# Optimization experiments

Hardware: AMD Instinct MI355X
Metric: run time of the kernel (lower is better)

## Reference

```python
import jax, jax.numpy as jnp
import numpy as np

MARGIN = 0.5


def _pairwise_dist(x):
    # Euclidean cdist via ||a||^2 + ||b||^2 - 2ab, with safe sqrt.
    sq = jnp.sum(x * x, axis=-1)  # (N,)
    d2 = sq[:, None] + sq[None, :] - 2.0 * (x @ x.T)
    d2 = jnp.maximum(d2, 0.0)
    return jnp.sqrt(jnp.where(d2 > 0.0, d2, 1.0)) * (d2 > 0.0)


def setup_inputs() -> dict:
    key = jax.random.key(0)
    k1, k2 = jax.random.split(key)
    N, D = 8192, 128
    embeddings = jax.random.normal(k1, (N, D), dtype=jnp.float32)
    labels = jax.random.randint(k2, (N,), 0, 7, dtype=jnp.int64)
    return {"embeddings": embeddings, "labels": labels}


def reference(embeddings, labels):
    N = embeddings.shape[0]
    dist = _pairwise_dist(embeddings)  # (N, N)
    same = labels[:, None] == labels[None, :]
    eye = jnp.eye(N, dtype=bool)
    pos_mask = same & ~eye
    neg_mask = ~same
    big = jnp.asarray(jnp.finfo(dist.dtype).max, dist.dtype)
    # hardest positive: max dist among same-label (excl. self)
    pos_dist = jnp.max(jnp.where(pos_mask, dist, -big), axis=1)
    # hardest negative: min dist among different-label
    neg_dist = jnp.min(jnp.where(neg_mask, dist, big), axis=1)
    valid = jnp.any(pos_mask, axis=1) & jnp.any(neg_mask, axis=1)
    per_row = jax.nn.relu(pos_dist - neg_dist + MARGIN)
    loss_sum = jnp.sum(jnp.where(valid, per_row, 0.0))
    count = jnp.sum(valid)
    return loss_sum / jnp.maximum(count, 1).astype(loss_sum.dtype)
```

## Files before the change

### kernel.cpp

```cpp
#include <hip/hip_runtime.h>

#define N 8192
#define D 128
#define MARGIN 0.5f
#define FLT_BIG 3.402823466e+38f

typedef __bf16 bf16x8 __attribute__((ext_vector_type(8)));
typedef float f32x4 __attribute__((ext_vector_type(4)));
typedef unsigned short u16x8 __attribute__((ext_vector_type(8)));

__device__ __forceinline__ unsigned short f2bf_rne(float f) {
  unsigned u = __float_as_uint(f);
  u += 0x7FFFu + ((u >> 16) & 1u);
  return (unsigned short)(u >> 16);
}

#define FRAG_OFF(tile, k, lane) ((size_t)(tile) * 2048 + (size_t)(k) * 512 + (size_t)(lane) * 8)

__global__ void k_prep(const float* __restrict__ x, const int* __restrict__ lab,
                       unsigned short* __restrict__ xb, float* __restrict__ sq,
                       unsigned* __restrict__ posw, unsigned* __restrict__ negw,
                       unsigned* __restrict__ hist, float* __restrict__ acc,
                       unsigned* __restrict__ ticket) {
  const int t = threadIdx.x;
  const int row = blockIdx.x * 16 + (t >> 4);
  const int c = t & 15;
  const float4 v0 = ((const float4*)x)[row * 32 + c * 2];
  const float4 v1 = ((const float4*)x)[row * 32 + c * 2 + 1];
  u16x8 o;
  o[0] = f2bf_rne(v0.x); o[1] = f2bf_rne(v0.y);
  o[2] = f2bf_rne(v0.z); o[3] = f2bf_rne(v0.w);
  o[4] = f2bf_rne(v1.x); o[5] = f2bf_rne(v1.y);
  o[6] = f2bf_rne(v1.z); o[7] = f2bf_rne(v1.w);
  *(u16x8*)(xb + FRAG_OFF(row >> 4, c >> 2, ((c & 3) * 16) + (row & 15))) = o;
  float s = v0.x * v0.x + v0.y * v0.y + v0.z * v0.z + v0.w * v0.w +
            v1.x * v1.x + v1.y * v1.y + v1.z * v1.z + v1.w * v1.w;
#pragma unroll
  for (int off = 1; off < 16; off <<= 1) s += __shfl_xor(s, off, 64);
  if (c == 0) {
    sq[row] = s;
    posw[row] = 0u;
    negw[row] = 0x7F800000u;
  }

  if (blockIdx.x == 0) {
    __shared__ unsigned h[8];
    if (t < 8) h[t] = 0u;
    __syncthreads();
    unsigned long long cA = 0ull, cB = 0ull;
#pragma unroll
    for (int it = 0; it < 32; ++it) {
      const int l = lab[t + it * 256] & 7;
      if (l < 4) cA += 1ull << (l * 16);
      else       cB += 1ull << ((l - 4) * 16);
    }
#pragma unroll
    for (int off = 1; off < 64; off <<= 1) {
      cA += __shfl_xor(cA, off, 64);
      cB += __shfl_xor(cB, off, 64);
    }
    if ((t & 63) == 0) {
#pragma unroll
      for (int q = 0; q < 4; ++q) {
        atomicAdd(&h[q],     (unsigned)((cA >> (q * 16)) & 0xFFFFu));
        atomicAdd(&h[4 + q], (unsigned)((cB >> (q * 16)) & 0xFFFFu));
      }
    }
    __syncthreads();
    if (t < 8) hist[t] = h[t];
    if (t == 0) { acc[0] = 0.f; acc[1] = 0.f; ticket[0] = 0u; }
  }
}

__global__ __launch_bounds__(256, 4) void k_mine(
    const unsigned short* __restrict__ xb, const float* __restrict__ sq,
    const int* __restrict__ lab, unsigned* __restrict__ posw, unsigned* __restrict__ negw) {
  const int t = threadIdx.x;
  const int w = t >> 6;
  const int lane = t & 63;
  const int col = lane & 15;
  const int quad = lane >> 4;
  const int i0 = blockIdx.x * 128 + w * 32;
  const int jbase = blockIdx.y * 256;

  bf16x8 a[2][4];
#pragma unroll
  for (int is = 0; is < 2; ++is)
#pragma unroll
    for (int k = 0; k < 4; ++k)
      a[is][k] = *(const bf16x8*)(xb + FRAG_OFF((i0 >> 4) + is, k, lane));

  int labi[2][4];
#pragma unroll
  for (int is = 0; is < 2; ++is)
#pragma unroll
    for (int r = 0; r < 4; ++r) labi[is][r] = lab[i0 + is * 16 + quad * 4 + r];

  float pos[2][4], neg[2][4];
#pragma unroll
  for (int is = 0; is < 2; ++is)
#pragma unroll
    for (int r = 0; r < 4; ++r) { pos[is][r] = -FLT_BIG; neg[is][r] = FLT_BIG; }

  const float* sqp = sq + jbase + col;
  const int* labp = lab + jbase + col;
  const unsigned short* gb = xb + FRAG_OFF(jbase >> 4, 0, lane);

  bf16x8 b0A, b1A, b2A, b3A, b0B, b1B, b2B, b3B;
  float sqjA, sqjB;
  int labjA, labjB;

#define LOADB(S, js_) do {                                        \
    const unsigned short* g = gb + (size_t)(js_) * 2048;          \
    b0##S = *(const bf16x8*)(g);                                  \
    b1##S = *(const bf16x8*)(g + 512);                            \
    b2##S = *(const bf16x8*)(g + 1024);                           \
    b3##S = *(const bf16x8*)(g + 1536);                           \
    sqj##S = sqp[(js_) * 16];                                     \
    labj##S = labp[(js_) * 16];                                   \
  } while (0)

#define COMPUTE(S) do {                                                        \
    f32x4 acc0 = {0.f, 0.f, 0.f, 0.f}, acc1 = {0.f, 0.f, 0.f, 0.f};           \
    acc0 = __builtin_amdgcn_mfma_f32_16x16x32_bf16(a[0][0], b0##S, acc0, 0, 0, 0); \
    acc1 = __builtin_amdgcn_mfma_f32_16x16x32_bf16(a[1][0], b0##S, acc1, 0, 0, 0); \
    acc0 = __builtin_amdgcn_mfma_f32_16x16x32_bf16(a[0][1], b1##S, acc0, 0, 0, 0); \
    acc1 = __builtin_amdgcn_mfma_f32_16x16x32_bf16(a[1][1], b1##S, acc1, 0, 0, 0); \
    acc0 = __builtin_amdgcn_mfma_f32_16x16x32_bf16(a[0][2], b2##S, acc0, 0, 0, 0); \
    acc1 = __builtin_amdgcn_mfma_f32_16x16x32_bf16(a[1][2], b2##S, acc1, 0, 0, 0); \
    acc0 = __builtin_amdgcn_mfma_f32_16x16x32_bf16(a[0][3], b3##S, acc0, 0, 0, 0); \
    acc1 = __builtin_amdgcn_mfma_f32_16x16x32_bf16(a[1][3], b3##S, acc1, 0, 0, 0); \
    _Pragma("unroll")                                                          \
    for (int r = 0; r < 4; ++r) {                                              \
      const float m0 = fmaf(-2.f, acc0[r], sqj##S);                            \
      const float m1 = fmaf(-2.f, acc1[r], sqj##S);                            \
      const bool s0 = (labi[0][r] == labj##S);                                 \
      const bool s1 = (labi[1][r] == labj##S);                                 \
      pos[0][r] = fmaxf(pos[0][r], s0 ? m0 : -FLT_BIG);                        \
      neg[0][r] = fminf(neg[0][r], s0 ? FLT_BIG : m0);                         \
      pos[1][r] = fmaxf(pos[1][r], s1 ? m1 : -FLT_BIG);                        \
      neg[1][r] = fminf(neg[1][r], s1 ? FLT_BIG : m1);                         \
    }                                                                          \
  } while (0)

  LOADB(A, 0);
#pragma unroll 1
  for (int js = 0; js < 14; js += 2) {
    LOADB(B, js + 1);
    COMPUTE(A);
    LOADB(A, js + 2);
    COMPUTE(B);
  }
  LOADB(B, 15);
  COMPUTE(A);
  COMPUTE(B);

#undef LOADB
#undef COMPUTE

#pragma unroll
  for (int is = 0; is < 2; ++is)
#pragma unroll
    for (int r = 0; r < 4; ++r) {
      float p = pos[is][r], n = neg[is][r];
#pragma unroll
      for (int off = 1; off < 16; off <<= 1) {
        p = fmaxf(p, __shfl_xor(p, off, 64));
        n = fminf(n, __shfl_xor(n, off, 64));
      }
      if (col == 0) {
        const int i = i0 + is * 16 + quad * 4 + r;
        const float sqi = sq[i];
        atomicMax(posw + i, __float_as_uint(fmaxf(sqi + p, 0.f)));
        atomicMin(negw + i, __float_as_uint(fmaxf(sqi + n, 0.f)));
      }
    }
}

__global__ void k_tail(const unsigned* __restrict__ posw, const unsigned* __restrict__ negw,
                       const int* __restrict__ lab, const unsigned* __restrict__ hist,
                       float* __restrict__ acc, unsigned* __restrict__ ticket,
                       float* __restrict__ out) {
  __shared__ float ls[4], cs[4];
  const int t = threadIdx.x;
  const int i = blockIdx.x * 256 + t;
  const float pd2 = __uint_as_float(posw[i]);
  const float nd2 = __uint_as_float(negw[i]);
  const unsigned cnt = hist[lab[i] & 7];
  const bool valid = (cnt >= 2u) && (cnt < (unsigned)N);
  float loss = 0.f, c = 0.f;
  if (valid) {
    loss = fmaxf(sqrtf(pd2) - sqrtf(fminf(nd2, FLT_BIG)) + MARGIN, 0.f);
    c = 1.f;
  }
#pragma unroll
  for (int off = 1; off < 64; off <<= 1) {
    loss += __shfl_xor(loss, off, 64);
    c += __shfl_xor(c, off, 64);
  }
  const int wv = t >> 6;
  if ((t & 63) == 0) { ls[wv] = loss; cs[wv] = c; }
  __syncthreads();
  if (t == 0) {
    atomicAdd(acc + 0, ls[0] + ls[1] + ls[2] + ls[3]);
    atomicAdd(acc + 1, cs[0] + cs[1] + cs[2] + cs[3]);
    __threadfence();
    const unsigned tk = atomicAdd(ticket, 1u);
    if (tk == 31u) {
      const float lsum = atomicAdd(acc + 0, 0.f);
      const float csum = atomicAdd(acc + 1, 0.f);
      out[0] = lsum / fmaxf(csum, 1.f);
    }
  }
}

extern "C" void kernel_launch(void* const* d_in, const int* in_sizes, int n_in,
                              void* d_out, int out_size, void* d_ws, size_t ws_size,
                              hipStream_t stream) {
  const float* x = (const float*)d_in[0];
  const int* lab = (const int*)d_in[1];
  char* ws = (char*)d_ws;
  unsigned short* xb = (unsigned short*)ws;
  float* sq = (float*)(ws + (size_t)N * D * 2);
  unsigned* posw = (unsigned*)((char*)sq + (size_t)N * 4);
  unsigned* negw = posw + N;
  unsigned* hist = negw + N;
  unsigned* ticket = hist + 8;
  float* acc = (float*)(ticket + 1);
  float* out = (float*)d_out;

  hipLaunchKernelGGL(k_prep, dim3(512), dim3(256), 0, stream, x, lab, xb, sq,
                     posw, negw, hist, acc, ticket);
  hipLaunchKernelGGL(k_mine, dim3(64, 32), dim3(256), 0, stream, xb, sq, lab, posw, negw);
  hipLaunchKernelGGL(k_tail, dim3(32), dim3(256), 0, stream, posw, negw, lab, hist,
                     acc, ticket, out);
}
```

Measured before the change: 100.2 us.

## Fuse tail reduction into mining kernel via last-block ticket; triple-buffer B loads

Removes the separate k_tail launch. The last k_mine block to finish, found with an atomic ticket counter, now reads all posw/negw values and computes the final loss. The B-fragment prefetch in the mining loop goes from double to triple buffering, putting loads further ahead of the MFMA compute. The costs are a serial 8192-element tail in one block and more registers, which could lower occupancy.

```diff
diff --git a/kernel.cpp b/kernel.cpp
--- a/kernel.cpp
+++ b/kernel.cpp
@@ -4,6 +4,7 @@
 #define D 128
 #define MARGIN 0.5f
 #define FLT_BIG 3.402823466e+38f
+#define NBLK 2048
 
 typedef __bf16 bf16x8 __attribute__((ext_vector_type(8)));
 typedef float f32x4 __attribute__((ext_vector_type(4)));
@@ -20,8 +21,7 @@
 __global__ void k_prep(const float* __restrict__ x, const int* __restrict__ lab,
                        unsigned short* __restrict__ xb, float* __restrict__ sq,
                        unsigned* __restrict__ posw, unsigned* __restrict__ negw,
-                       unsigned* __restrict__ hist, float* __restrict__ acc,
-                       unsigned* __restrict__ ticket) {
+                       unsigned* __restrict__ hist, unsigned* __restrict__ ticket) {
   const int t = threadIdx.x;
   const int row = blockIdx.x * 16 + (t >> 4);
   const int c = t & 15;
@@ -68,13 +68,18 @@
     }
     __syncthreads();
     if (t < 8) hist[t] = h[t];
-    if (t == 0) { acc[0] = 0.f; acc[1] = 0.f; ticket[0] = 0u; }
+    if (t == 0) ticket[0] = 0u;
   }
 }
 
 __global__ __launch_bounds__(256, 4) void k_mine(
     const unsigned short* __restrict__ xb, const float* __restrict__ sq,
-    const int* __restrict__ lab, unsigned* __restrict__ posw, unsigned* __restrict__ negw) {
+    const int* __restrict__ lab, unsigned* __restrict__ posw, unsigned* __restrict__ negw,
+    const unsigned* __restrict__ hist, unsigned* __restrict__ ticket,
+    float* __restrict__ out) {
+  __shared__ float ls[4], cs[4];
+  __shared__ unsigned lastf;
+
   const int t = threadIdx.x;
   const int w = t >> 6;
   const int lane = t & 63;
@@ -106,9 +111,9 @@
   const int* labp = lab + jbase + col;
   const unsigned short* gb = xb + FRAG_OFF(jbase >> 4, 0, lane);
 
-  bf16x8 b0A, b1A, b2A, b3A, b0B, b1B, b2B, b3B;
-  float sqjA, sqjB;
-  int labjA, labjB;
+  bf16x8 b0A, b1A, b2A, b3A, b0B, b1B, b2B, b3B, b0C, b1C, b2C, b3C;
+  float sqjA, sqjB, sqjC;
+  int labjA, labjB, labjC;
 
 #define LOADB(S, js_) do {                                        \
     const unsigned short* g = gb + (size_t)(js_) * 2048;          \
@@ -144,16 +149,22 @@
   } while (0)
 
   LOADB(A, 0);
+  LOADB(B, 1);
 #pragma unroll 1
-  for (int js = 0; js < 14; js += 2) {
-    LOADB(B, js + 1);
+  for (int js = 0; js < 12; js += 3) {
+    LOADB(C, js + 2);
     COMPUTE(A);
-    LOADB(A, js + 2);
+    LOADB(A, js + 3);
     COMPUTE(B);
-  }
-  LOADB(B, 15);
+    LOADB(B, js + 4);
+    COMPUTE(C);
+  }
+  LOADB(C, 14);
   COMPUTE(A);
+  LOADB(A, 15);
   COMPUTE(B);
+  COMPUTE(C);
+  COMPUTE(A);
 
 #undef LOADB
 #undef COMPUTE
@@ -175,43 +186,37 @@
         atomicMin(negw + i, __float_as_uint(fmaxf(sqi + n, 0.f)));
       }
     }
-}
-
-__global__ void k_tail(const unsigned* __restrict__ posw, const unsigned* __restrict__ negw,
-                       const int* __restrict__ lab, const unsigned* __restrict__ hist,
-                       float* __restrict__ acc, unsigned* __restrict__ ticket,
-                       float* __restrict__ out) {
-  __shared__ float ls[4], cs[4];
-  const int t = threadIdx.x;
-  const int i = blockIdx.x * 256 + t;
-  const float pd2 = __uint_as_float(posw[i]);
-  const float nd2 = __uint_as_float(negw[i]);
-  const unsigned cnt = hist[lab[i] & 7];
-  const bool valid = (cnt >= 2u) && (cnt < (unsigned)N);
-  float loss = 0.f, c = 0.f;
-  if (valid) {
-    loss = fmaxf(sqrtf(pd2) - sqrtf(fminf(nd2, FLT_BIG)) + MARGIN, 0.f);
-    c = 1.f;
+
+  __syncthreads();
+  __threadfence();
+  if (t == 0) lastf = (atomicAdd(ticket, 1u) == (unsigned)(NBLK - 1)) ? 1u : 0u;
+  __syncthreads();
+  if (!lastf) return;
+
+  float loss = 0.f, cnt = 0.f;
+#pragma unroll 4
+  for (int it = 0; it < 32; ++it) {
+    const int i = t + it * 256;
+    const float pd2 = __uint_as_float(
+        __hip_atomic_load(posw + i, __ATOMIC_RELAXED, __HIP_MEMORY_SCOPE_AGENT));
+    const float nd2 = __uint_as_float(
+        __hip_atomic_load(negw + i, __ATOMIC_RELAXED, __HIP_MEMORY_SCOPE_AGENT));
+    const unsigned c = hist[lab[i] & 7];
+    if (c >= 2u && c < (unsigned)N) {
+      loss += fmaxf(sqrtf(pd2) - sqrtf(fminf(nd2, FLT_BIG)) + MARGIN, 0.f);
+      cnt += 1.f;
+    }
   }
 #pragma unroll
   for (int off = 1; off < 64; off <<= 1) {
     loss += __shfl_xor(loss, off, 64);
-    c += __shfl_xor(c, off, 64);
-  }
-  const int wv = t >> 6;
-  if ((t & 63) == 0) { ls[wv] = loss; cs[wv] = c; }
+    cnt += __shfl_xor(cnt, off, 64);
+  }
+  if (lane == 0) { ls[w] = loss; cs[w] = cnt; }
   __syncthreads();
-  if (t == 0) {
-    atomicAdd(acc + 0, ls[0] + ls[1] + ls[2] + ls[3]);
-    atomicAdd(acc + 1, cs[0] + cs[1] + cs[2] + cs[3]);
-    __threadfence();
-    const unsigned tk = atomicAdd(ticket, 1u);
-    if (tk == 31u) {
-      const float lsum = atomicAdd(acc + 0, 0.f);
-      const float csum = atomicAdd(acc + 1, 0.f);
-      out[0] = lsum / fmaxf(csum, 1.f);
-    }
-  }
+  if (t == 0)
+    out[0] = (ls[0] + ls[1] + ls[2] + ls[3]) /
+             fmaxf(cs[0] + cs[1] + cs[2] + cs[3], 1.f);
 }
 
 extern "C" void kernel_launch(void* const* d_in, const int* in_sizes, int n_in,
@@ -226,12 +231,10 @@
   unsigned* negw = posw + N;
   unsigned* hist = negw + N;
   unsigned* ticket = hist + 8;
-  float* acc = (float*)(ticket + 1);
   float* out = (float*)d_out;
 
   hipLaunchKernelGGL(k_prep, dim3(512), dim3(256), 0, stream, x, lab, xb, sq,
-                     posw, negw, hist, acc, ticket);
-  hipLaunchKernelGGL(k_mine, dim3(64, 32), dim3(256), 0, stream, xb, sq, lab, posw, negw);
-  hipLaunchKernelGGL(k_tail, dim3(32), dim3(256), 0, stream, posw, negw, lab, hist,
-                     acc, ticket, out);
-}
+                     posw, negw, hist, ticket);
+  hipLaunchKernelGGL(k_mine, dim3(64, 32), dim3(256), 0, stream, xb, sq, lab,
+                     posw, negw, hist, ticket, out);
+}
```

Result: slower. 339.3 us (+238.7%).

## Exploit distance matrix symmetry by computing only lower-triangular block tiles

Applied to the files above, without the earlier changes.

The mining kernel now launches only the block tiles on or below the diagonal (1056 instead of 2048) and, for off-diagonal tiles, also reduces each tile column-wise. The column reduction goes through shared-memory atomics on order-preserving float keys, and the result is scattered to the column rows' global pos/neg words. This roughly halves the MFMA and distance work. In exchange it adds per-tile shuffles, LDS atomics and extra global atomics, and the triangular index decode costs a sqrt.

```diff
diff --git a/kernel.cpp b/kernel.cpp
--- a/kernel.cpp
+++ b/kernel.cpp
@@ -4,6 +4,7 @@
 #define D 128
 #define MARGIN 0.5f
 #define FLT_BIG 3.402823466e+38f
+#define NBLK 1056
 
 typedef __bf16 bf16x8 __attribute__((ext_vector_type(8)));
 typedef float f32x4 __attribute__((ext_vector_type(4)));
@@ -13,6 +14,15 @@
   unsigned u = __float_as_uint(f);
   u += 0x7FFFu + ((u >> 16) & 1u);
   return (unsigned short)(u >> 16);
+}
+
+__device__ __forceinline__ unsigned fkey(float f) {
+  unsigned u = __float_as_uint(f);
+  return ((int)u < 0) ? ~u : (u | 0x80000000u);
+}
+__device__ __forceinline__ float fkey_inv(unsigned k) {
+  unsigned u = ((int)k < 0) ? (k & 0x7FFFFFFFu) : ~k;
+  return __uint_as_float(u);
 }
 
 #define FRAG_OFF(tile, k, lane) ((size_t)(tile) * 2048 + (size_t)(k) * 512 + (size_t)(lane) * 8)
@@ -72,16 +82,35 @@
   }
 }
 
-__global__ __launch_bounds__(256, 4) void k_mine(
+__global__ __launch_bounds__(256)
+__attribute__((amdgpu_waves_per_eu(4, 4)))
+void k_mine(
     const unsigned short* __restrict__ xb, const float* __restrict__ sq,
     const int* __restrict__ lab, unsigned* __restrict__ posw, unsigned* __restrict__ negw) {
+  __shared__ unsigned cposk[256], cnegk[256];
+
   const int t = threadIdx.x;
   const int w = t >> 6;
   const int lane = t & 63;
   const int col = lane & 15;
   const int quad = lane >> 4;
-  const int i0 = blockIdx.x * 128 + w * 32;
-  const int jbase = blockIdx.y * 256;
+
+  int bj, bi;
+  {
+    const int T = blockIdx.x;
+    int b = (int)((sqrtf((float)(4 * T + 1)) - 1.0f) * 0.5f);
+    while (b * (b + 1) > T) --b;
+    while ((b + 1) * (b + 2) <= T) ++b;
+    bj = b;
+    bi = T - b * (b + 1);
+  }
+  const bool diag = ((bi >> 1) == bj);
+  const int i0 = bi * 128 + w * 32;
+  const int jbase = bj * 256;
+
+  cposk[t] = 0u;
+  cnegk[t] = 0xFFFFFFFFu;
+  __syncthreads();
 
   bf16x8 a[2][4];
 #pragma unroll
@@ -91,10 +120,15 @@
       a[is][k] = *(const bf16x8*)(xb + FRAG_OFF((i0 >> 4) + is, k, lane));
 
   int labi[2][4];
-#pragma unroll
-  for (int is = 0; is < 2; ++is)
-#pragma unroll
-    for (int r = 0; r < 4; ++r) labi[is][r] = lab[i0 + is * 16 + quad * 4 + r];
+  float sqi[2][4];
+#pragma unroll
+  for (int is = 0; is < 2; ++is)
+#pragma unroll
+    for (int r = 0; r < 4; ++r) {
+      const int i = i0 + is * 16 + quad * 4 + r;
+      labi[is][r] = lab[i];
+      sqi[is][r] = sq[i];
+    }
 
   float pos[2][4], neg[2][4];
 #pragma unroll
@@ -120,7 +154,7 @@
     labj##S = labp[(js_) * 16];                                   \
   } while (0)
 
-#define COMPUTE(S) do {                                                        \
+#define COMPUTE(S, js_) do {                                                   \
     f32x4 acc0 = {0.f, 0.f, 0.f, 0.f}, acc1 = {0.f, 0.f, 0.f, 0.f};           \
     acc0 = __builtin_amdgcn_mfma_f32_16x16x32_bf16(a[0][0], b0##S, acc0, 0, 0, 0); \
     acc1 = __builtin_amdgcn_mfma_f32_16x16x32_bf16(a[1][0], b0##S, acc1, 0, 0, 0); \
@@ -130,6 +164,7 @@
     acc1 = __builtin_amdgcn_mfma_f32_16x16x32_bf16(a[1][2], b2##S, acc1, 0, 0, 0); \
     acc0 = __builtin_amdgcn_mfma_f32_16x16x32_bf16(a[0][3], b3##S, acc0, 0, 0, 0); \
     acc1 = __builtin_amdgcn_mfma_f32_16x16x32_bf16(a[1][3], b3##S, acc1, 0, 0, 0); \
+    float cp = -FLT_BIG, cn = FLT_BIG;                                         \
     _Pragma("unroll")                                                          \
     for (int r = 0; r < 4; ++r) {                                              \
       const float m0 = fmaf(-2.f, acc0[r], sqj##S);                            \
@@ -140,6 +175,24 @@
       neg[0][r] = fminf(neg[0][r], s0 ? FLT_BIG : m0);                         \
       pos[1][r] = fmaxf(pos[1][r], s1 ? m1 : -FLT_BIG);                        \
       neg[1][r] = fminf(neg[1][r], s1 ? FLT_BIG : m1);                         \
+      if (!diag) {                                                             \
+        const float mc0 = fmaf(-2.f, acc0[r], sqi[0][r]);                      \
+        const float mc1 = fmaf(-2.f, acc1[r], sqi[1][r]);                      \
+        cp = fmaxf(cp, s0 ? mc0 : -FLT_BIG);                                   \
+        cn = fminf(cn, s0 ? FLT_BIG : mc0);                                    \
+        cp = fmaxf(cp, s1 ? mc1 : -FLT_BIG);                                   \
+        cn = fminf(cn, s1 ? FLT_BIG : mc1);                                    \
+      }                                                                        \
+    }                                                                          \
+    if (!diag) {                                                               \
+      cp = fmaxf(cp, __shfl_xor(cp, 16, 64));                                  \
+      cp = fmaxf(cp, __shfl_xor(cp, 32, 64));                                  \
+      cn = fminf(cn, __shfl_xor(cn, 16, 64));                                  \
+      cn = fminf(cn, __shfl_xor(cn, 32, 64));                                  \
+      if (quad == 0) {                                                         \
+        atomicMax(&cposk[(js_) * 16 + col], fkey(cp));                         \
+        atomicMin(&cnegk[(js_) * 16 + col], fkey(cn));                         \
+      }                                                                        \
     }                                                                          \
   } while (0)
 
@@ -147,13 +200,13 @@
 #pragma unroll 1
   for (int js = 0; js < 14; js += 2) {
     LOADB(B, js + 1);
-    COMPUTE(A);
+    COMPUTE(A, js);
     LOADB(A, js + 2);
-    COMPUTE(B);
+    COMPUTE(B, js + 1);
   }
   LOADB(B, 15);
-  COMPUTE(A);
-  COMPUTE(B);
+  COMPUTE(A, 14);
+  COMPUTE(B, 15);
 
 #undef LOADB
 #undef COMPUTE
@@ -170,11 +223,20 @@
       }
       if (col == 0) {
         const int i = i0 + is * 16 + quad * 4 + r;
-        const float sqi = sq[i];
-        atomicMax(posw + i, __float_as_uint(fmaxf(sqi + p, 0.f)));
-        atomicMin(negw + i, __float_as_uint(fmaxf(sqi + n, 0.f)));
+        atomicMax(posw + i, __float_as_uint(fmaxf(sqi[is][r] + p, 0.f)));
+        atomicMin(negw + i, __float_as_uint(fmaxf(sqi[is][r] + n, 0.f)));
       }
     }
+
+  if (!diag) {
+    __syncthreads();
+    const int j = jbase + t;
+    const float cpv = fkey_inv(cposk[t]);
+    const float cnv = fkey_inv(cnegk[t]);
+    const float sqj = sq[j];
+    atomicMax(posw + j, __float_as_uint(fmaxf(sqj + cpv, 0.f)));
+    atomicMin(negw + j, __float_as_uint(fmaxf(sqj + cnv, 0.f)));
+  }
 }
 
 __global__ void k_tail(const unsigned* __restrict__ posw, const unsigned* __restrict__ negw,
@@ -231,7 +293,7 @@
 
   hipLaunchKernelGGL(k_prep, dim3(512), dim3(256), 0, stream, x, lab, xb, sq,
                      posw, negw, hist, acc, ticket);
-  hipLaunchKernelGGL(k_mine, dim3(64, 32), dim3(256), 0, stream, xb, sq, lab, posw, negw);
+  hipLaunchKernelGGL(k_mine, dim3(NBLK), dim3(256), 0, stream, xb, sq, lab, posw, negw);
   hipLaunchKernelGGL(k_tail, dim3(32), dim3(256), 0, stream, posw, negw, lab, hist,
                      acc, ticket, out);
 }
```

After: 97.81 us (median of 3 runs). 2.4% less time.
